# Kernel tuning notes

Hardware: AMD Instinct MI355X
Metric: run time of the kernel (lower is better)

Reference implementation:

```python
import jax, jax.numpy as jnp
import numpy as np

EPS = 1e-6  # F.normalize eps

N, C, H, W = 2, 64, 64, 64
HEADS, DK, DV = 2, 64, 32


def setup_inputs() -> dict:
    key = jax.random.key(0)
    ks = jax.random.split(key, 9)
    w = lambda k, sh: jax.random.normal(k, sh, jnp.float32) * 0.05
    return {
        "x":  jax.random.normal(ks[0], (N, C, H, W), jnp.float32),
        "Wq": w(ks[1], (HEADS, DK, C)), "bq": w(ks[2], (HEADS, DK)),
        "Wk": w(ks[3], (HEADS, DK, C)), "bk": w(ks[4], (HEADS, DK)),
        "Wv": w(ks[5], (HEADS, DV, C)), "bv": w(ks[6], (HEADS, DV)),
        "Wm": w(ks[7], (C, HEADS * DV)), "bm": w(ks[8], (C,)),
    }


def _l2norm(t):
    # F.normalize(dim=1) on [N, dk, L]; here heads are stacked: [N, h, dk, L], axis=2
    n = jnp.linalg.norm(t, axis=2, keepdims=True)
    return t / jnp.maximum(n, EPS)


def reference(x, Wq, bq, Wk, bk, Wv, bv, Wm, bm):
    n, c, h, w = x.shape
    L = h * w
    xf = x.reshape(n, c, L)  # 1x1 conv == pointwise channel GEMM; x_enc = x (no pos enc)
    Q = jnp.einsum('hkc,ncl->nhkl', Wq, xf) + bq[None, :, :, None]
    K = jnp.einsum('hkc,ncl->nhkl', Wk, xf) + bk[None, :, :, None]
    V = jnp.einsum('hvc,ncl->nhvl', Wv, xf) + bv[None, :, :, None]
    Q = _l2norm(Q)
    K = _l2norm(K)
    # cosine-similarity attention: contract over dk, softmax over keys
    A = jax.nn.softmax(jnp.einsum('nhkl,nhkm->nhlm', Q, K), axis=-1)  # [n,h,L,L]
    R = jnp.einsum('nhlm,nhvm->nhvl', A, V)  # [n,h,dv,L]
    Rc = R.reshape(n, -1, L)  # concat heads along channels
    out = jnp.einsum('oc,ncl->nol', Wm, Rc) + bm[None, :, None]
    return out.reshape(n, c, h, w) + x  # residual
```

## Files before the change

kernel.cpp:

```cpp
#include <hip/hip_runtime.h>
#include <cmath>


typedef __bf16 bf16x8 __attribute__((ext_vector_type(8)));
typedef __bf16 bf16x4 __attribute__((ext_vector_type(4)));
typedef float f4_t __attribute__((ext_vector_type(4)));

#define LQ 4096
#define NH 4
#define KS 8

__device__ inline f4_t mfma16(bf16x8 a, bf16x8 b, f4_t c) {
    return __builtin_amdgcn_mfma_f32_16x16x32_bf16(a, b, c, 0, 0, 0);
}

__device__ inline bf16x8 cvt8(const float* p) {
    f4_t a = *(const f4_t*)p, b = *(const f4_t*)(p + 4);
    bf16x8 r;
    r[0] = (__bf16)a[0]; r[1] = (__bf16)a[1]; r[2] = (__bf16)a[2]; r[3] = (__bf16)a[3];
    r[4] = (__bf16)b[0]; r[5] = (__bf16)b[1]; r[6] = (__bf16)b[2]; r[7] = (__bf16)b[3];
    return r;
}

__global__ __launch_bounds__(256) void k1_qkv(
        const float* __restrict__ x,
        const float* __restrict__ Wq, const float* __restrict__ bq,
        const float* __restrict__ Wk, const float* __restrict__ bk,
        const float* __restrict__ Wv, const float* __restrict__ bv,
        __bf16* __restrict__ Qb, __bf16* __restrict__ Kb,
        __bf16* __restrict__ Vtb) {
    const int tid  = threadIdx.x;
    const int lane = tid & 63;
    const int w    = tid >> 6;
    const int quad = lane >> 4;
    const int l15  = lane & 15;
    const int lt   = blockIdx.x;
    const int n    = blockIdx.y;
    const int l0   = lt * 32;

    __shared__ __bf16 xl[32][72];

    {
        const int c0 = tid >> 5, l = tid & 31;
#pragma unroll
        for (int i = 0; i < 8; ++i) {
            const int c = c0 + i * 8;
            xl[l][c] = (__bf16)x[((size_t)n * 64 + c) * LQ + l0 + l];
        }
    }

    const float* Wqk = (w < 2) ? Wq : Wk;
    const float* bqk = (w < 2) ? bq : bk;
    const int h = w & 1;

    bf16x8 af[4][2], av[2];
#pragma unroll
    for (int t = 0; t < 4; ++t)
#pragma unroll
        for (int kh = 0; kh < 2; ++kh)
            af[t][kh] = cvt8(Wqk + (size_t)(h * 64 + t * 16 + l15) * 64
                                  + kh * 32 + quad * 8);
#pragma unroll
    for (int kh = 0; kh < 2; ++kh)
        av[kh] = cvt8(Wv + (size_t)(w * 16 + l15) * 64 + kh * 32 + quad * 8);

    f4_t binit[4], bvinit;
#pragma unroll
    for (int t = 0; t < 4; ++t)
#pragma unroll
        for (int r = 0; r < 4; ++r)
            binit[t][r] = bqk[h * 64 + t * 16 + quad * 4 + r];
#pragma unroll
    for (int r = 0; r < 4; ++r)
        bvinit[r] = bv[w * 16 + quad * 4 + r];

    __syncthreads();

    f4_t acc[4][2], vacc[2];
#pragma unroll
    for (int lsub = 0; lsub < 2; ++lsub) {
        bf16x8 bf0 = *(const bf16x8*)&xl[lsub * 16 + l15][quad * 8];
        bf16x8 bf1 = *(const bf16x8*)&xl[lsub * 16 + l15][32 + quad * 8];
#pragma unroll
        for (int t = 0; t < 4; ++t) {
            f4_t a = mfma16(af[t][0], bf0, binit[t]);
            acc[t][lsub] = mfma16(af[t][1], bf1, a);
        }
        f4_t va = mfma16(av[0], bf0, bvinit);
        vacc[lsub] = mfma16(av[1], bf1, va);
    }

    const int nh = n * 2 + h;
    __bf16* dst  = (w < 2) ? Qb : Kb;
    const float post = (w < 2) ? 1.44269504f : 1.0f;
#pragma unroll
    for (int lsub = 0; lsub < 2; ++lsub) {
        float ss = 0.f;
#pragma unroll
        for (int t = 0; t < 4; ++t)
#pragma unroll
            for (int r = 0; r < 4; ++r)
                ss = fmaf(acc[t][lsub][r], acc[t][lsub][r], ss);
        ss += __shfl_xor(ss, 16, 64);
        ss += __shfl_xor(ss, 32, 64);
        const float rn = post / fmaxf(sqrtf(ss), 1e-6f);

        const int l = l0 + lsub * 16 + l15;
#pragma unroll
        for (int t = 0; t < 4; ++t) {
            bf16x4 pk;
#pragma unroll
            for (int r = 0; r < 4; ++r) pk[r] = (__bf16)(acc[t][lsub][r] * rn);
            const int kc = t * 2 + (quad >> 1);
            *(bf16x4*)(dst + ((size_t)(nh * 8 + kc) * LQ + l) * 8 + (quad & 1) * 4) = pk;
        }
#pragma unroll
        for (int r = 0; r < 4; ++r) {
            const int vrow = w * 16 + quad * 4 + r;
            Vtb[(size_t)(n * 64 + vrow) * LQ + l] = (__bf16)vacc[lsub][r];
        }
    }
}

__global__ __launch_bounds__(256, 4) void k2_attn(
        const __bf16* __restrict__ Qb, const __bf16* __restrict__ Kb,
        const __bf16* __restrict__ Vtb,
        __bf16* __restrict__ numPb, float* __restrict__ denP) {
    const int tid  = threadIdx.x;
    const int lane = tid & 63;
    const int wave = tid >> 6;
    const int quad = lane >> 4;
    const int l15  = lane & 15;
    const int nh   = blockIdx.y;
    const int ks   = blockIdx.z;
    const int qbase = blockIdx.x * 128 + wave * 32;
    const int kbase = ks * 512;

    __shared__ __bf16 Kl[2][4096];
    __shared__ __bf16 P[4][2][16][72];

    const f4_t fzero = {0.f, 0.f, 0.f, 0.f};

    const __bf16* s_src0, * s_src1;
    {
        const int s0 = tid, s1 = tid + 256;
        const int kc0 = ((s0 >> 6) & 1) * 4 + ((s0 >> 4) & 3);
        const int ll0 = (s0 >> 7) * 16 + (s0 & 15);
        const int kc1 = ((s1 >> 6) & 1) * 4 + ((s1 >> 4) & 3);
        const int ll1 = (s1 >> 7) * 16 + (s1 & 15);
        s_src0 = Kb + ((size_t)(nh * 8 + kc0) * LQ + kbase + ll0) * 8;
        s_src1 = Kb + ((size_t)(nh * 8 + kc1) * LQ + kbase + ll1) * 8;
    }

    bf16x8 qf[2][2];
#pragma unroll
    for (int qt = 0; qt < 2; ++qt)
#pragma unroll
        for (int kh = 0; kh < 2; ++kh)
            qf[qt][kh] = *(const bf16x8*)(Qb +
                ((size_t)(nh * 8 + kh * 4 + quad) * LQ + qbase + qt * 16 + l15) * 8);

    f4_t racc[2][2];
#pragma unroll
    for (int a = 0; a < 2; ++a)
#pragma unroll
        for (int b = 0; b < 2; ++b) racc[a][b] = fzero;
    float den[2] = {0.f, 0.f};

    const __bf16* v_src = Vtb + (size_t)(nh * 32 + l15) * LQ + kbase + quad * 8;

    *(bf16x8*)&Kl[0][(size_t)tid * 8]         = *(const bf16x8*)s_src0;
    *(bf16x8*)&Kl[0][(size_t)(tid + 256) * 8] = *(const bf16x8*)s_src1;
    __syncthreads();

#pragma unroll 2
    for (int ch = 0; ch < 8; ++ch) {
        const int cur = ch & 1;

        if (ch < 7) {
            *(bf16x8*)&Kl[cur ^ 1][(size_t)tid * 8] =
                *(const bf16x8*)(s_src0 + (size_t)(ch + 1) * 512);
            *(bf16x8*)&Kl[cur ^ 1][(size_t)(tid + 256) * 8] =
                *(const bf16x8*)(s_src1 + (size_t)(ch + 1) * 512);
        }

        bf16x8 vf[2][2];
#pragma unroll
        for (int vt = 0; vt < 2; ++vt)
#pragma unroll
            for (int kp = 0; kp < 2; ++kp)
                vf[vt][kp] = *(const bf16x8*)(v_src + (size_t)vt * 16 * LQ
                                              + ch * 64 + kp * 32);

#pragma unroll
        for (int ktp = 0; ktp < 2; ++ktp) {
            bf16x8 kf[2][2];
#pragma unroll
            for (int i = 0; i < 2; ++i)
#pragma unroll
                for (int kh = 0; kh < 2; ++kh)
                    kf[i][kh] = *(const bf16x8*)
                        &Kl[cur][(size_t)((ktp * 2 + i) * 128 + kh * 64
                                          + quad * 16 + l15) * 8];

            f4_t s[2][2];
#pragma unroll
            for (int qt = 0; qt < 2; ++qt)
#pragma unroll
                for (int i = 0; i < 2; ++i) {
                    f4_t t = mfma16(kf[i][0], qf[qt][0], fzero);
                    s[qt][i] = mfma16(kf[i][1], qf[qt][1], t);
                }

#pragma unroll
            for (int qt = 0; qt < 2; ++qt)
#pragma unroll
                for (int i = 0; i < 2; ++i) {
                    bf16x4 pv;
                    float d = 0.f;
#pragma unroll
                    for (int r = 0; r < 4; ++r) {
                        float p = __builtin_exp2f(s[qt][i][r]);
                        d += p;
                        pv[r] = (__bf16)p;
                    }
                    den[qt] += d;
                    *(bf16x4*)&P[wave][qt][l15][(ktp * 2 + i) * 16 + quad * 4] = pv;
                }
        }

#pragma unroll
        for (int qt = 0; qt < 2; ++qt)
#pragma unroll
            for (int kp = 0; kp < 2; ++kp) {
                bf16x8 pf = *(const bf16x8*)&P[wave][qt][l15][kp * 32 + quad * 8];
                racc[0][qt] = mfma16(vf[0][kp], pf, racc[0][qt]);
                racc[1][qt] = mfma16(vf[1][kp], pf, racc[1][qt]);
            }

        __syncthreads();
    }

#pragma unroll
    for (int qt = 0; qt < 2; ++qt) {
        den[qt] += __shfl_xor(den[qt], 16, 64);
        den[qt] += __shfl_xor(den[qt], 32, 64);
    }

    const size_t pb = (size_t)(nh * KS + ks) * LQ;
#pragma unroll
    for (int vt = 0; vt < 2; ++vt)
#pragma unroll
        for (int qt = 0; qt < 2; ++qt) {
            bf16x4 pk;
#pragma unroll
            for (int r = 0; r < 4; ++r) pk[r] = (__bf16)racc[vt][qt][r];
            *(bf16x4*)(numPb + (pb + qbase + qt * 16 + l15) * 32
                             + vt * 16 + quad * 4) = pk;
        }

    if (lane < 16)
#pragma unroll
        for (int qt = 0; qt < 2; ++qt)
            denP[pb + qbase + qt * 16 + lane] = den[qt];
}

__global__ __launch_bounds__(256) void k3_out(
        const __bf16* __restrict__ numPb, const float* __restrict__ denP,
        const float* __restrict__ Wm, const float* __restrict__ bm,
        const float* __restrict__ x, float* __restrict__ out) {
    const int tid = threadIdx.x;
    const int lt  = blockIdx.x;
    const int n   = blockIdx.y;
    const int l0  = lt * 16;

    __shared__ float Rps[2][64][17];
    __shared__ float dinv[2][16];

    if (tid < 32) {
        const int hh = tid >> 4, li = tid & 15;
        float s = 0.f;
#pragma unroll
        for (int k = 0; k < KS; ++k)
            s += denP[(size_t)((n * 2 + hh) * KS + k) * LQ + l0 + li];
        dinv[hh][li] = 1.0f / s;
    }

    {
        const int vg = tid & 3, l = (tid >> 2) & 15;
        const int hh = (tid >> 6) & 1, sh = tid >> 7;
        const size_t base = (size_t)(n * 2 + hh) * KS * LQ;
        float a[8] = {0.f, 0.f, 0.f, 0.f, 0.f, 0.f, 0.f, 0.f};
#pragma unroll
        for (int k = 0; k < 4; ++k) {
            const int kk = sh * 4 + k;
            bf16x8 v8 = *(const bf16x8*)(numPb +
                (base + (size_t)kk * LQ + l0 + l) * 32 + vg * 8);
#pragma unroll
            for (int j = 0; j < 8; ++j) a[j] += (float)v8[j];
        }
#pragma unroll
        for (int j = 0; j < 8; ++j)
            Rps[sh][hh * 32 + vg * 8 + j][l] = a[j];
    }
    __syncthreads();

    const int l = tid & 15, og = tid >> 4;
    const float d0 = dinv[0][l], d1 = dinv[1][l];
    float rj[64];
#pragma unroll
    for (int j = 0; j < 64; ++j)
        rj[j] = (Rps[0][j][l] + Rps[1][j][l]) * (j < 32 ? d0 : d1);

#pragma unroll
    for (int oi = 0; oi < 4; ++oi) {
        const int o = og * 4 + oi;
        const float* wr = Wm + (size_t)o * 64;
        float a = bm[o];
#pragma unroll
        for (int j4 = 0; j4 < 16; ++j4) {
            f4_t t = *(const f4_t*)(wr + j4 * 4);
            a = fmaf(t[0], rj[j4 * 4 + 0], a);
            a = fmaf(t[1], rj[j4 * 4 + 1], a);
            a = fmaf(t[2], rj[j4 * 4 + 2], a);
            a = fmaf(t[3], rj[j4 * 4 + 3], a);
        }
        const size_t idx = (size_t)(n * 64 + o) * LQ + l0 + l;
        out[idx] = a + x[idx];
    }
}

extern "C" void kernel_launch(void* const* d_in, const int* in_sizes, int n_in,
                              void* d_out, int out_size, void* d_ws, size_t ws_size,
                              hipStream_t stream) {
    const float* x  = (const float*)d_in[0];
    const float* Wq = (const float*)d_in[1];
    const float* bq = (const float*)d_in[2];
    const float* Wk = (const float*)d_in[3];
    const float* bk = (const float*)d_in[4];
    const float* Wv = (const float*)d_in[5];
    const float* bv = (const float*)d_in[6];
    const float* Wm = (const float*)d_in[7];
    const float* bm = (const float*)d_in[8];
    float* out = (float*)d_out;

    __bf16* Qb    = (__bf16*)d_ws;
    __bf16* Kb    = Qb + (size_t)NH * LQ * 64;
    __bf16* Vtb   = Kb + (size_t)NH * LQ * 64;
    __bf16* numPb = Vtb + (size_t)NH * 32 * LQ;
    float*  denP  = (float*)(numPb + (size_t)NH * KS * LQ * 32);

    k1_qkv<<<dim3(128, 2), dim3(256), 0, stream>>>(x, Wq, bq, Wk, bk, Wv, bv,
                                                   Qb, Kb, Vtb);
    k2_attn<<<dim3(32, NH, KS), dim3(256), 0, stream>>>(Qb, Kb, Vtb, numPb, denP);
    k3_out<<<dim3(256, 2), dim3(256), 0, stream>>>(numPb, denP, Wm, bm, x, out);
}
```

Measured before the change: 112.1 us.

## Halve QKV tile, reorder attention grid, prefetch K two chunks ahead via registers

The QKV projection kernel now handles 16 positions per block instead of 32, doubling its grid so more CUs are busy. The attention kernel's grid is reordered so the key-split index varies fastest, which groups blocks sharing Q tiles and may change cache locality. K tiles are now loaded into registers two chunks ahead of their LDS store, so global-load latency can overlap compute. This raises register use, and the unroll pragma was dropped.

```diff
diff --git a/kernel.cpp b/kernel.cpp
--- a/kernel.cpp
+++ b/kernel.cpp
@@ -36,15 +36,15 @@
     const int l15  = lane & 15;
     const int lt   = blockIdx.x;
     const int n    = blockIdx.y;
-    const int l0   = lt * 32;
-
-    __shared__ __bf16 xl[32][72];
-
-    {
-        const int c0 = tid >> 5, l = tid & 31;
-#pragma unroll
-        for (int i = 0; i < 8; ++i) {
-            const int c = c0 + i * 8;
+    const int l0   = lt * 16;
+
+    __shared__ __bf16 xl[16][72];
+
+    {
+        const int l = tid & 15, c0 = tid >> 4;
+#pragma unroll
+        for (int i = 0; i < 4; ++i) {
+            const int c = c0 * 4 + i;
             xl[l][c] = (__bf16)x[((size_t)n * 64 + c) * LQ + l0 + l];
         }
     }
@@ -76,48 +76,46 @@
 
     __syncthreads();
 
-    f4_t acc[4][2], vacc[2];
-#pragma unroll
-    for (int lsub = 0; lsub < 2; ++lsub) {
-        bf16x8 bf0 = *(const bf16x8*)&xl[lsub * 16 + l15][quad * 8];
-        bf16x8 bf1 = *(const bf16x8*)&xl[lsub * 16 + l15][32 + quad * 8];
+    f4_t acc[4], vacc;
+    {
+        bf16x8 bf0 = *(const bf16x8*)&xl[l15][quad * 8];
+        bf16x8 bf1 = *(const bf16x8*)&xl[l15][32 + quad * 8];
 #pragma unroll
         for (int t = 0; t < 4; ++t) {
             f4_t a = mfma16(af[t][0], bf0, binit[t]);
-            acc[t][lsub] = mfma16(af[t][1], bf1, a);
+            acc[t] = mfma16(af[t][1], bf1, a);
         }
         f4_t va = mfma16(av[0], bf0, bvinit);
-        vacc[lsub] = mfma16(av[1], bf1, va);
+        vacc = mfma16(av[1], bf1, va);
     }
 
     const int nh = n * 2 + h;
     __bf16* dst  = (w < 2) ? Qb : Kb;
     const float post = (w < 2) ? 1.44269504f : 1.0f;
-#pragma unroll
-    for (int lsub = 0; lsub < 2; ++lsub) {
+    {
         float ss = 0.f;
 #pragma unroll
         for (int t = 0; t < 4; ++t)
 #pragma unroll
             for (int r = 0; r < 4; ++r)
-                ss = fmaf(acc[t][lsub][r], acc[t][lsub][r], ss);
+                ss = fmaf(acc[t][r], acc[t][r], ss);
         ss += __shfl_xor(ss, 16, 64);
         ss += __shfl_xor(ss, 32, 64);
         const float rn = post / fmaxf(sqrtf(ss), 1e-6f);
 
-        const int l = l0 + lsub * 16 + l15;
+        const int l = l0 + l15;
 #pragma unroll
         for (int t = 0; t < 4; ++t) {
             bf16x4 pk;
 #pragma unroll
-            for (int r = 0; r < 4; ++r) pk[r] = (__bf16)(acc[t][lsub][r] * rn);
+            for (int r = 0; r < 4; ++r) pk[r] = (__bf16)(acc[t][r] * rn);
             const int kc = t * 2 + (quad >> 1);
             *(bf16x4*)(dst + ((size_t)(nh * 8 + kc) * LQ + l) * 8 + (quad & 1) * 4) = pk;
         }
 #pragma unroll
         for (int r = 0; r < 4; ++r) {
             const int vrow = w * 16 + quad * 4 + r;
-            Vtb[(size_t)(n * 64 + vrow) * LQ + l] = (__bf16)vacc[lsub][r];
+            Vtb[(size_t)(n * 64 + vrow) * LQ + l] = (__bf16)vacc[r];
         }
     }
 }
@@ -131,9 +129,9 @@
     const int wave = tid >> 6;
     const int quad = lane >> 4;
     const int l15  = lane & 15;
-    const int nh   = blockIdx.y;
-    const int ks   = blockIdx.z;
-    const int qbase = blockIdx.x * 128 + wave * 32;
+    const int ks   = blockIdx.x;
+    const int nh   = blockIdx.z;
+    const int qbase = blockIdx.y * 128 + wave * 32;
     const int kbase = ks * 512;
 
     __shared__ __bf16 Kl[2][4096];
@@ -169,19 +167,26 @@
 
     const __bf16* v_src = Vtb + (size_t)(nh * 32 + l15) * LQ + kbase + quad * 8;
 
-    *(bf16x8*)&Kl[0][(size_t)tid * 8]         = *(const bf16x8*)s_src0;
-    *(bf16x8*)&Kl[0][(size_t)(tid + 256) * 8] = *(const bf16x8*)s_src1;
+    {
+        bf16x8 r0 = *(const bf16x8*)s_src0;
+        bf16x8 r1 = *(const bf16x8*)s_src1;
+        *(bf16x8*)&Kl[0][(size_t)tid * 8]         = r0;
+        *(bf16x8*)&Kl[0][(size_t)(tid + 256) * 8] = r1;
+    }
+    bf16x8 rg0 = *(const bf16x8*)(s_src0 + 512);
+    bf16x8 rg1 = *(const bf16x8*)(s_src1 + 512);
     __syncthreads();
 
-#pragma unroll 2
     for (int ch = 0; ch < 8; ++ch) {
         const int cur = ch & 1;
 
+        const int pf = (ch < 6) ? ch + 2 : 7;
+        bf16x8 rg0n = *(const bf16x8*)(s_src0 + (size_t)pf * 512);
+        bf16x8 rg1n = *(const bf16x8*)(s_src1 + (size_t)pf * 512);
+
         if (ch < 7) {
-            *(bf16x8*)&Kl[cur ^ 1][(size_t)tid * 8] =
-                *(const bf16x8*)(s_src0 + (size_t)(ch + 1) * 512);
-            *(bf16x8*)&Kl[cur ^ 1][(size_t)(tid + 256) * 8] =
-                *(const bf16x8*)(s_src1 + (size_t)(ch + 1) * 512);
+            *(bf16x8*)&Kl[cur ^ 1][(size_t)tid * 8]         = rg0;
+            *(bf16x8*)&Kl[cur ^ 1][(size_t)(tid + 256) * 8] = rg1;
         }
 
         bf16x8 vf[2][2];
@@ -233,12 +238,14 @@
         for (int qt = 0; qt < 2; ++qt)
 #pragma unroll
             for (int kp = 0; kp < 2; ++kp) {
-                bf16x8 pf = *(const bf16x8*)&P[wave][qt][l15][kp * 32 + quad * 8];
-                racc[0][qt] = mfma16(vf[0][kp], pf, racc[0][qt]);
-                racc[1][qt] = mfma16(vf[1][kp], pf, racc[1][qt]);
+                bf16x8 pf8 = *(const bf16x8*)&P[wave][qt][l15][kp * 32 + quad * 8];
+                racc[0][qt] = mfma16(vf[0][kp], pf8, racc[0][qt]);
+                racc[1][qt] = mfma16(vf[1][kp], pf8, racc[1][qt]);
             }
 
         __syncthreads();
+        rg0 = rg0n;
+        rg1 = rg1n;
     }
 
 #pragma unroll
@@ -350,8 +357,8 @@
     __bf16* numPb = Vtb + (size_t)NH * 32 * LQ;
     float*  denP  = (float*)(numPb + (size_t)NH * KS * LQ * 32);
 
-    k1_qkv<<<dim3(128, 2), dim3(256), 0, stream>>>(x, Wq, bq, Wk, bk, Wv, bv,
+    k1_qkv<<<dim3(256, 2), dim3(256), 0, stream>>>(x, Wq, bq, Wk, bk, Wv, bv,
                                                    Qb, Kb, Vtb);
-    k2_attn<<<dim3(32, NH, KS), dim3(256), 0, stream>>>(Qb, Kb, Vtb, numPb, denP);
+    k2_attn<<<dim3(KS, 32, NH), dim3(256), 0, stream>>>(Qb, Kb, Vtb, numPb, denP);
     k3_out<<<dim3(256, 2), dim3(256), 0, stream>>>(numPb, denP, Wm, bm, x, out);
 }
```

Result: slower. 114.5 us (+2.1%).
